# Kernel optimization log

Hardware: AMD Instinct MI355X
Metric: run time of the kernel (lower is better)

The kernel has to match this reference:

```python
import jax, jax.numpy as jnp
import numpy as np

ITERATION = 10

def setup_inputs() -> dict:
    key = jax.random.key(0)
    k1, k2, k3 = jax.random.split(key, 3)
    a_inter = jax.random.normal(k1, (8, 64, 64, 32, 32), dtype=jnp.float32)
    logits = jax.random.normal(k2, (8, 64), dtype=jnp.float32)
    W = jax.random.normal(k3, (1, 64, 64), dtype=jnp.float32)
    return {"a_inter": a_inter, "logits": logits, "W": W}


def reference(a_inter, logits, W):
    N = W.shape[1]  # num_nodes
    B = a_inter.shape[0]
    # feats: [B, N, C*H*W]
    feats = a_inter[:, :, :N, :, :].reshape(B, N, -1)
    # expand logits [B, N] -> [B, N, N] (unsqueeze(1).expand in torch)
    logits0 = jnp.broadcast_to(logits[:, None, :], (B, N, N))

    feats_norm = jnp.linalg.norm(feats, ord=2, axis=2, keepdims=True)  # [B, N, 1]
    pairwise_norm = feats_norm @ jnp.swapaxes(feats_norm, 1, 2)        # [B, N, N]
    pairwise_dot = feats @ jnp.swapaxes(feats, 1, 2)                   # [B, N, N]
    pairwise_sim = pairwise_dot / (pairwise_norm + 1e-6)
    W_sym = (W + jnp.swapaxes(W, 1, 2)) / 2.0
    pairwise_potential = pairwise_sim * W_sym                          # [B, N, N]

    unary_potential = logits0

    def body(i, l):
        probs = jnp.swapaxes(jax.nn.sigmoid(l), 1, 2)  # [B, N, N]
        # probs*pp - (1-probs)*pp == (2*probs - 1)*pp
        pp_E = jnp.sum((2.0 * probs - 1.0) * pairwise_potential, axis=2, keepdims=True)
        return unary_potential + pp_E

    logits_out = jax.lax.fori_loop(0, ITERATION, body, logits0)
    return logits_out.mean(axis=1)  # [B, N]
```

## Files before the change

### kernel.cpp

```cpp
#include <hip/hip_runtime.h>
#include <math.h>

#define BATCH 8
#define NN 64
#define DD 65536
#define BPB 64
#define NBLK (BATCH * BPB)
#define KC (DD / BPB)
#define KW (KC / 4)
#define KSTEPS (KW / 32)
#define NTRI 10
#define PSZ (NTRI * 256)
#define GRAM_FLOATS (BATCH * PSZ)
#define INIT_N (GRAM_FLOATS + BATCH)

typedef float  floatx4 __attribute__((ext_vector_type(4)));
typedef __bf16 bf16x8  __attribute__((ext_vector_type(8)));

static __device__ __forceinline__ bf16x8 cvt8(float4 lo, float4 hi) {
    const unsigned sel = 0x07060302u;
    union { unsigned u[4]; bf16x8 v; } r;
    r.u[0] = __builtin_amdgcn_perm(__float_as_uint(lo.y), __float_as_uint(lo.x), sel);
    r.u[1] = __builtin_amdgcn_perm(__float_as_uint(lo.w), __float_as_uint(lo.z), sel);
    r.u[2] = __builtin_amdgcn_perm(__float_as_uint(hi.y), __float_as_uint(hi.x), sel);
    r.u[3] = __builtin_amdgcn_perm(__float_as_uint(hi.w), __float_as_uint(hi.z), sel);
    return r.v;
}

__global__ __launch_bounds__(256) void init_kernel(float* __restrict__ g) {
    int i = blockIdx.x * 256 + threadIdx.x;
    if (i < INIT_N) g[i] = 0.0f;
}

__global__ __launch_bounds__(256, 3) void fused_kernel(const float* __restrict__ a,
                                                       const float* __restrict__ logits,
                                                       const float* __restrict__ Wm,
                                                       float* __restrict__ gram,
                                                       float* __restrict__ out) {
    __shared__ __align__(16) union {
        float red[3][NTRI][64][4];
        struct {
            float G[NN][NN + 1];
            float E[NN];
            float nrm[NN];
            float part[4 * NN];
        } crf;
    } sh;
    __shared__ int lastFlag;

    const int bid = blockIdx.x;
    const int b = bid >> 6;
    const int c = bid & (BPB - 1);

    const int tid  = threadIdx.x;
    const int w    = tid >> 6;
    const int lane = tid & 63;
    const int m    = lane & 15;
    const int q    = lane >> 4;

    const float* base = a + (size_t)b * NN * DD + (size_t)c * KC + (size_t)w * KW
                          + (size_t)m * DD + q * 8;
    const float* p0 = base;
    const float* p1 = base + (size_t)16 * DD;
    const float* p2 = base + (size_t)32 * DD;
    const float* p3 = base + (size_t)48 * DD;

    floatx4 acc[NTRI];
    #pragma unroll
    for (int i = 0; i < NTRI; ++i) acc[i] = (floatx4)0.0f;

    float4 A0, A1, A2, A3, A4, A5, A6, A7;
    float4 B0, B1, B2, B3, B4, B5, B6, B7;

#define LOADSET(R0,R1,R2,R3,R4,R5,R6,R7, o)                                \
    R0 = *(const float4*)(p0 + (o));  R1 = *(const float4*)(p0 + (o) + 4); \
    R2 = *(const float4*)(p1 + (o));  R3 = *(const float4*)(p1 + (o) + 4); \
    R4 = *(const float4*)(p2 + (o));  R5 = *(const float4*)(p2 + (o) + 4); \
    R6 = *(const float4*)(p3 + (o));  R7 = *(const float4*)(p3 + (o) + 4);

#define MFMASET(R0,R1,R2,R3,R4,R5,R6,R7)                                   \
    {                                                                      \
        bf16x8 f0 = cvt8(R0, R1);                                          \
        bf16x8 f1 = cvt8(R2, R3);                                          \
        bf16x8 f2 = cvt8(R4, R5);                                          \
        bf16x8 f3 = cvt8(R6, R7);                                          \
        acc[0] = __builtin_amdgcn_mfma_f32_16x16x32_bf16(f0, f0, acc[0], 0, 0, 0); \
        acc[1] = __builtin_amdgcn_mfma_f32_16x16x32_bf16(f0, f1, acc[1], 0, 0, 0); \
        acc[2] = __builtin_amdgcn_mfma_f32_16x16x32_bf16(f0, f2, acc[2], 0, 0, 0); \
        acc[3] = __builtin_amdgcn_mfma_f32_16x16x32_bf16(f0, f3, acc[3], 0, 0, 0); \
        acc[4] = __builtin_amdgcn_mfma_f32_16x16x32_bf16(f1, f1, acc[4], 0, 0, 0); \
        acc[5] = __builtin_amdgcn_mfma_f32_16x16x32_bf16(f1, f2, acc[5], 0, 0, 0); \
        acc[6] = __builtin_amdgcn_mfma_f32_16x16x32_bf16(f1, f3, acc[6], 0, 0, 0); \
        acc[7] = __builtin_amdgcn_mfma_f32_16x16x32_bf16(f2, f2, acc[7], 0, 0, 0); \
        acc[8] = __builtin_amdgcn_mfma_f32_16x16x32_bf16(f2, f3, acc[8], 0, 0, 0); \
        acc[9] = __builtin_amdgcn_mfma_f32_16x16x32_bf16(f3, f3, acc[9], 0, 0, 0); \
    }

    LOADSET(A0,A1,A2,A3,A4,A5,A6,A7, 0)
    #pragma unroll
    for (int s = 0; s < KSTEPS; s += 2) {
        LOADSET(B0,B1,B2,B3,B4,B5,B6,B7, (s + 1) * 32)
        MFMASET(A0,A1,A2,A3,A4,A5,A6,A7)
        if (s + 2 < KSTEPS) { LOADSET(A0,A1,A2,A3,A4,A5,A6,A7, (s + 2) * 32) }
        MFMASET(B0,B1,B2,B3,B4,B5,B6,B7)
    }
#undef LOADSET
#undef MFMASET

    if (w > 0) {
        #pragma unroll
        for (int t = 0; t < NTRI; ++t)
            *(floatx4*)&sh.red[w - 1][t][lane][0] = acc[t];
    }
    __syncthreads();
    if (w == 0) {
        #pragma unroll
        for (int t = 0; t < NTRI; ++t) {
            floatx4 r0 = *(const floatx4*)&sh.red[0][t][lane][0];
            floatx4 r1 = *(const floatx4*)&sh.red[1][t][lane][0];
            floatx4 r2 = *(const floatx4*)&sh.red[2][t][lane][0];
            acc[t] += (r0 + r1) + r2;
        }
        float* pg = gram + (size_t)b * PSZ;
        #pragma unroll
        for (int t = 0; t < NTRI; ++t) {
            float* tp = pg + t * 256 + m;
            #pragma unroll
            for (int r = 0; r < 4; ++r)
                atomicAdd(&tp[(q * 4 + r) * 16], acc[t][r]);
        }
        __threadfence();
    }
    if (tid == 0) {
        unsigned* cnt = (unsigned*)(gram + GRAM_FLOATS);
        unsigned old = atomicAdd(cnt + b, 1u);
        lastFlag = (old == BPB - 1) ? 1 : 0;
    }
    __syncthreads();
    if (!lastFlag) return;

    const float* gb = gram + (size_t)b * PSZ;
    for (int idx = tid; idx < NN * NN; idx += 256) {
        int i  = idx >> 6, j = idx & 63;
        int ti = i >> 4, tj = j >> 4;
        int ib = ti <= tj ? ti : tj;
        int jb = ti <= tj ? tj : ti;
        int slot = ib * 4 - (ib * (ib - 1)) / 2 + (jb - ib);
        int rr = (ti <= tj) ? (i & 15) : (j & 15);
        int cc = (ti <= tj) ? (j & 15) : (i & 15);
        float v = __hip_atomic_load(gb + slot * 256 + rr * 16 + cc,
                                    __ATOMIC_RELAXED, __HIP_MEMORY_SCOPE_AGENT);
        sh.crf.G[i][j] = v;
    }
    __syncthreads();

    const int ci = tid & 63;
    const int jq = tid >> 6;

    if (jq == 0) sh.crf.nrm[ci] = sqrtf(sh.crf.G[ci][ci]);
    sh.crf.E[ci] = 0.0f;
    __syncthreads();

    const float ni = sh.crf.nrm[ci];
    #pragma unroll
    for (int jj = 0; jj < 16; ++jj) {
        int j = jq * 16 + jj;
        float wsym = 0.5f * (Wm[ci * NN + j] + Wm[j * NN + ci]);
        sh.crf.G[ci][j] = sh.crf.G[ci][j] / (ni * sh.crf.nrm[j] + 1e-6f) * wsym;
    }
    const float li = logits[b * NN + ci];
    __syncthreads();

    for (int it = 0; it < 10; ++it) {
        float acc2 = 0.0f;
        #pragma unroll
        for (int jj = 0; jj < 16; ++jj) {
            int j = jq * 16 + jj;
            float t = li + sh.crf.E[j];
            float s = 1.0f / (1.0f + expf(-t));
            acc2 = fmaf(2.0f * s - 1.0f, sh.crf.G[ci][j], acc2);
        }
        sh.crf.part[jq * NN + ci] = acc2;
        __syncthreads();
        if (jq == 0)
            sh.crf.E[ci] = sh.crf.part[ci] + sh.crf.part[NN + ci]
                         + sh.crf.part[2 * NN + ci] + sh.crf.part[3 * NN + ci];
        __syncthreads();
    }

    if (tid < 64) {
        float s = sh.crf.E[tid];
        for (int off = 32; off > 0; off >>= 1) s += __shfl_down(s, off);
        float meanE = __shfl(s, 0) * (1.0f / 64.0f);
        out[b * NN + tid] = logits[b * NN + tid] + meanE;
    }
}

extern "C" void kernel_launch(void* const* d_in, const int* in_sizes, int n_in,
                              void* d_out, int out_size, void* d_ws, size_t ws_size,
                              hipStream_t stream) {
    const float* a      = (const float*)d_in[0];
    const float* logits = (const float*)d_in[1];
    const float* Wm     = (const float*)d_in[2];
    float* out  = (float*)d_out;

    float* gram = (float*)d_ws;

    init_kernel<<<(INIT_N + 255) / 256, 256, 0, stream>>>(gram);
    fused_kernel<<<NBLK, 256, 0, stream>>>(a, logits, Wm, gram, out);
}
```

Baseline: 235.6 us.

## Stage feature tiles through LDS via async global_load_lds and drop gram atomics

The main loop now streams 64x32 float tiles into per-wave double-buffered LDS with global_load_lds and a swizzled layout, then reads MFMA operands from LDS. Previously each lane issued strided global float4 loads straight into registers. Gram partials are now written per block to a workspace buffer without atomics, and the last block of each batch reduces all 64 partials. This also shrinks the init kernel to clearing only the counters. In exchange, occupancy drops from 3 to 2 blocks per CU, and the last block performs a serial reduction over 64 partial tiles.

```diff
diff --git a/kernel.cpp b/kernel.cpp
--- a/kernel.cpp
+++ b/kernel.cpp
@@ -8,11 +8,11 @@
 #define NBLK (BATCH * BPB)
 #define KC (DD / BPB)
 #define KW (KC / 4)
-#define KSTEPS (KW / 32)
+#define BKF 32
+#define NT (KW / BKF)
+#define TILEF (NN * BKF)
 #define NTRI 10
 #define PSZ (NTRI * 256)
-#define GRAM_FLOATS (BATCH * PSZ)
-#define INIT_N (GRAM_FLOATS + BATCH)
 
 typedef float  floatx4 __attribute__((ext_vector_type(4)));
 typedef __bf16 bf16x8  __attribute__((ext_vector_type(8)));
@@ -27,26 +27,28 @@
     return r.v;
 }
 
-__global__ __launch_bounds__(256) void init_kernel(float* __restrict__ g) {
-    int i = blockIdx.x * 256 + threadIdx.x;
-    if (i < INIT_N) g[i] = 0.0f;
-}
-
-__global__ __launch_bounds__(256, 3) void fused_kernel(const float* __restrict__ a,
+__global__ __launch_bounds__(64) void init_kernel(unsigned* __restrict__ cnt) {
+    if (threadIdx.x < BATCH) cnt[threadIdx.x] = 0u;
+}
+
+__global__ __launch_bounds__(256, 2) void fused_kernel(const float* __restrict__ a,
                                                        const float* __restrict__ logits,
                                                        const float* __restrict__ Wm,
-                                                       float* __restrict__ gram,
+                                                       float* __restrict__ part,
+                                                       unsigned* __restrict__ cnt,
                                                        float* __restrict__ out) {
     __shared__ __align__(16) union {
+        float stage[4][2][TILEF];
         float red[3][NTRI][64][4];
         struct {
+            int   lastFlag;
+            float tri[PSZ];
             float G[NN][NN + 1];
             float E[NN];
             float nrm[NN];
-            float part[4 * NN];
+            float part4[4 * NN];
         } crf;
     } sh;
-    __shared__ int lastFlag;
 
     const int bid = blockIdx.x;
     const int b = bid >> 6;
@@ -58,32 +60,43 @@
     const int m    = lane & 15;
     const int q    = lane >> 4;
 
-    const float* base = a + (size_t)b * NN * DD + (size_t)c * KC + (size_t)w * KW
-                          + (size_t)m * DD + q * 8;
-    const float* p0 = base;
-    const float* p1 = base + (size_t)16 * DD;
-    const float* p2 = base + (size_t)32 * DD;
-    const float* p3 = base + (size_t)48 * DD;
+    const int    srow = lane >> 3;
+    const int    scol = ((((lane & 7) << 4) ^ (srow << 4)) >> 2);
+    const float* gs = a + (size_t)b * NN * DD + (size_t)srow * DD
+                        + (size_t)c * KC + (size_t)w * KW + scol;
+    float* ldsW = &sh.stage[w][0][0];
+
+    const int s1  = (m & 7) << 4;
+    const int loF = ((q << 5) ^ s1) >> 2;
+    const int hiF = (((q << 5) + 16) ^ s1) >> 2;
 
     floatx4 acc[NTRI];
     #pragma unroll
     for (int i = 0; i < NTRI; ++i) acc[i] = (floatx4)0.0f;
 
-    float4 A0, A1, A2, A3, A4, A5, A6, A7;
-    float4 B0, B1, B2, B3, B4, B5, B6, B7;
-
-#define LOADSET(R0,R1,R2,R3,R4,R5,R6,R7, o)                                \
-    R0 = *(const float4*)(p0 + (o));  R1 = *(const float4*)(p0 + (o) + 4); \
-    R2 = *(const float4*)(p1 + (o));  R3 = *(const float4*)(p1 + (o) + 4); \
-    R4 = *(const float4*)(p2 + (o));  R5 = *(const float4*)(p2 + (o) + 4); \
-    R6 = *(const float4*)(p3 + (o));  R7 = *(const float4*)(p3 + (o) + 4);
-
-#define MFMASET(R0,R1,R2,R3,R4,R5,R6,R7)                                   \
-    {                                                                      \
-        bf16x8 f0 = cvt8(R0, R1);                                          \
-        bf16x8 f1 = cvt8(R2, R3);                                          \
-        bf16x8 f2 = cvt8(R4, R5);                                          \
-        bf16x8 f3 = cvt8(R6, R7);                                          \
+#define STAGE(buf, t)                                                         \
+    { _Pragma("unroll")                                                       \
+      for (int i_ = 0; i_ < 8; ++i_)                                          \
+          __builtin_amdgcn_global_load_lds(                                   \
+              (const __attribute__((address_space(1))) void*)(gs + (size_t)i_ * 8 * DD + (t) * BKF), \
+              (__attribute__((address_space(3))) void*)(ldsW + (buf) * TILEF + i_ * 256),            \
+              16, 0, 0); }
+
+#define COMPUTE(buf)                                                          \
+    {                                                                         \
+        const float* tb = ldsW + (buf) * TILEF;                               \
+        float4 l0 = *(const float4*)(tb + (m     ) * BKF + loF);              \
+        float4 h0 = *(const float4*)(tb + (m     ) * BKF + hiF);              \
+        float4 l1 = *(const float4*)(tb + (m + 16) * BKF + loF);              \
+        float4 h1 = *(const float4*)(tb + (m + 16) * BKF + hiF);              \
+        float4 l2 = *(const float4*)(tb + (m + 32) * BKF + loF);              \
+        float4 h2 = *(const float4*)(tb + (m + 32) * BKF + hiF);              \
+        float4 l3 = *(const float4*)(tb + (m + 48) * BKF + loF);              \
+        float4 h3 = *(const float4*)(tb + (m + 48) * BKF + hiF);              \
+        bf16x8 f0 = cvt8(l0, h0);                                             \
+        bf16x8 f1 = cvt8(l1, h1);                                             \
+        bf16x8 f2 = cvt8(l2, h2);                                             \
+        bf16x8 f3 = cvt8(l3, h3);                                             \
         acc[0] = __builtin_amdgcn_mfma_f32_16x16x32_bf16(f0, f0, acc[0], 0, 0, 0); \
         acc[1] = __builtin_amdgcn_mfma_f32_16x16x32_bf16(f0, f1, acc[1], 0, 0, 0); \
         acc[2] = __builtin_amdgcn_mfma_f32_16x16x32_bf16(f0, f2, acc[2], 0, 0, 0); \
@@ -96,17 +109,24 @@
         acc[9] = __builtin_amdgcn_mfma_f32_16x16x32_bf16(f3, f3, acc[9], 0, 0, 0); \
     }
 
-    LOADSET(A0,A1,A2,A3,A4,A5,A6,A7, 0)
+    STAGE(0, 0)
+    STAGE(1, 1)
     #pragma unroll
-    for (int s = 0; s < KSTEPS; s += 2) {
-        LOADSET(B0,B1,B2,B3,B4,B5,B6,B7, (s + 1) * 32)
-        MFMASET(A0,A1,A2,A3,A4,A5,A6,A7)
-        if (s + 2 < KSTEPS) { LOADSET(A0,A1,A2,A3,A4,A5,A6,A7, (s + 2) * 32) }
-        MFMASET(B0,B1,B2,B3,B4,B5,B6,B7)
-    }
-#undef LOADSET
-#undef MFMASET
-
+    for (int t = 0; t < NT; ++t) {
+        if (t < NT - 1) { asm volatile("s_waitcnt vmcnt(8)" ::: "memory"); }
+        else            { asm volatile("s_waitcnt vmcnt(0)" ::: "memory"); }
+        __builtin_amdgcn_sched_barrier(0);
+        COMPUTE(t & 1)
+        if (t + 2 < NT) {
+            asm volatile("s_waitcnt lgkmcnt(0)" ::: "memory");
+            __builtin_amdgcn_sched_barrier(0);
+            STAGE(t & 1, t + 2)
+        }
+    }
+#undef STAGE
+#undef COMPUTE
+
+    __syncthreads();
     if (w > 0) {
         #pragma unroll
         for (int t = 0; t < NTRI; ++t)
@@ -121,25 +141,49 @@
             floatx4 r2 = *(const floatx4*)&sh.red[2][t][lane][0];
             acc[t] += (r0 + r1) + r2;
         }
-        float* pg = gram + (size_t)b * PSZ;
+        float* pg = part + (size_t)bid * PSZ;
         #pragma unroll
         for (int t = 0; t < NTRI; ++t) {
             float* tp = pg + t * 256 + m;
             #pragma unroll
             for (int r = 0; r < 4; ++r)
-                atomicAdd(&tp[(q * 4 + r) * 16], acc[t][r]);
+                tp[(q * 4 + r) * 16] = acc[t][r];
         }
         __threadfence();
     }
     if (tid == 0) {
-        unsigned* cnt = (unsigned*)(gram + GRAM_FLOATS);
         unsigned old = atomicAdd(cnt + b, 1u);
-        lastFlag = (old == BPB - 1) ? 1 : 0;
-    }
-    __syncthreads();
-    if (!lastFlag) return;
-
-    const float* gb = gram + (size_t)b * PSZ;
+        sh.crf.lastFlag = (old == BPB - 1) ? 1 : 0;
+    }
+    __syncthreads();
+    if (!sh.crf.lastFlag) return;
+
+    __threadfence();
+
+    const float* pb = part + (size_t)b * BPB * PSZ;
+    for (int fo = tid; fo < PSZ / 4; fo += 256) {
+        float4 a0 = {0.f, 0.f, 0.f, 0.f}, a1 = a0, a2 = a0, a3 = a0;
+        const float* p = pb + fo * 4;
+        #pragma unroll 4
+        for (int cc2 = 0; cc2 < BPB; cc2 += 4) {
+            float4 v0 = *(const float4*)(p + (size_t)(cc2 + 0) * PSZ);
+            float4 v1 = *(const float4*)(p + (size_t)(cc2 + 1) * PSZ);
+            float4 v2 = *(const float4*)(p + (size_t)(cc2 + 2) * PSZ);
+            float4 v3 = *(const float4*)(p + (size_t)(cc2 + 3) * PSZ);
+            a0.x += v0.x; a0.y += v0.y; a0.z += v0.z; a0.w += v0.w;
+            a1.x += v1.x; a1.y += v1.y; a1.z += v1.z; a1.w += v1.w;
+            a2.x += v2.x; a2.y += v2.y; a2.z += v2.z; a2.w += v2.w;
+            a3.x += v3.x; a3.y += v3.y; a3.z += v3.z; a3.w += v3.w;
+        }
+        float4 s;
+        s.x = (a0.x + a1.x) + (a2.x + a3.x);
+        s.y = (a0.y + a1.y) + (a2.y + a3.y);
+        s.z = (a0.z + a1.z) + (a2.z + a3.z);
+        s.w = (a0.w + a1.w) + (a2.w + a3.w);
+        *(float4*)&sh.crf.tri[fo * 4] = s;
+    }
+    __syncthreads();
+
     for (int idx = tid; idx < NN * NN; idx += 256) {
         int i  = idx >> 6, j = idx & 63;
         int ti = i >> 4, tj = j >> 4;
@@ -148,9 +192,7 @@
         int slot = ib * 4 - (ib * (ib - 1)) / 2 + (jb - ib);
         int rr = (ti <= tj) ? (i & 15) : (j & 15);
         int cc = (ti <= tj) ? (j & 15) : (i & 15);
-        float v = __hip_atomic_load(gb + slot * 256 + rr * 16 + cc,
-                                    __ATOMIC_RELAXED, __HIP_MEMORY_SCOPE_AGENT);
-        sh.crf.G[i][j] = v;
+        sh.crf.G[i][j] = sh.crf.tri[slot * 256 + rr * 16 + cc];
     }
     __syncthreads();
 
@@ -180,11 +222,11 @@
             float s = 1.0f / (1.0f + expf(-t));
             acc2 = fmaf(2.0f * s - 1.0f, sh.crf.G[ci][j], acc2);
         }
-        sh.crf.part[jq * NN + ci] = acc2;
+        sh.crf.part4[jq * NN + ci] = acc2;
         __syncthreads();
         if (jq == 0)
-            sh.crf.E[ci] = sh.crf.part[ci] + sh.crf.part[NN + ci]
-                         + sh.crf.part[2 * NN + ci] + sh.crf.part[3 * NN + ci];
+            sh.crf.E[ci] = sh.crf.part4[ci] + sh.crf.part4[NN + ci]
+                         + sh.crf.part4[2 * NN + ci] + sh.crf.part4[3 * NN + ci];
         __syncthreads();
     }
 
@@ -204,8 +246,9 @@
     const float* Wm     = (const float*)d_in[2];
     float* out  = (float*)d_out;
 
-    float* gram = (float*)d_ws;
-
-    init_kernel<<<(INIT_N + 255) / 256, 256, 0, stream>>>(gram);
-    fused_kernel<<<NBLK, 256, 0, stream>>>(a, logits, Wm, gram, out);
-}
+    float*    part = (float*)d_ws;
+    unsigned* cnt  = (unsigned*)(part + (size_t)NBLK * PSZ);
+
+    init_kernel<<<1, 64, 0, stream>>>(cnt);
+    fused_kernel<<<NBLK, 256, 0, stream>>>(a, logits, Wm, part, cnt, out);
+}
```

Measured after the change: 251.3 us. +6.7%, slower.
